# Optimization experiments

Measured on AMD Instinct MI355X. Metric: run time of the kernel, lower is better.

Reference implementation:

```python
import jax, jax.numpy as jnp
import numpy as np
from jax import lax

CAPACITY_FACTOR = 1.0

def setup_inputs() -> dict:
    key = jax.random.key(0)
    k1, k2 = jax.random.split(key)
    x = jax.random.normal(k1, (16384, 4096), dtype=jnp.float32)
    wg = jax.random.normal(k2, (128, 4096), dtype=jnp.float32) * (1.0 / np.sqrt(4096))
    return {"x": x, "wg": wg}


def reference(x, wg):
    # logits: [T, E]
    logits = jnp.einsum('td,ed->te', x, wg)
    T, E = logits.shape
    capacity = 2 * int(CAPACITY_FACTOR * ((T + E - 1) // E))  # static python int

    # top-2 expert indices per token
    _, top2 = lax.top_k(logits, 2)           # [T, 2]
    idx1, idx2 = top2[:, 0], top2[:, 1]       # [T]

    mask1 = jax.nn.one_hot(idx1, E, dtype=jnp.int32)  # [T, E]
    mask2 = jax.nn.one_hot(idx2, E, dtype=jnp.int32)

    gates = jax.nn.softmax(logits, axis=1)    # [T, E]
    gates1_s = jnp.sum(gates * mask1, axis=1)  # [T]
    gates2_s = jnp.sum(gates * mask2, axis=1)

    # per-expert running position (cumsum over tokens)
    locations1 = jnp.cumsum(mask1, axis=0) - 1
    locations2 = jnp.cumsum(mask2, axis=0) - 1 + jnp.sum(mask1, axis=0, keepdims=True)

    # drop tokens over capacity
    mask1 = mask1 * (locations1 < capacity).astype(jnp.int32)
    mask2 = mask2 * (locations2 < capacity).astype(jnp.int32)

    locations1_s = jnp.sum(locations1 * mask1, axis=1)  # [T]
    locations2_s = jnp.sum(locations2 * mask2, axis=1)

    # load-balancing aux loss (float32 branch of original)
    me = jnp.sum(gates, axis=0)                       # [E]
    ce = jnp.sum(mask1.astype(gates.dtype), axis=0)   # [E] (post-capacity mask)
    l_aux = jnp.sum(me * ce) * (E / (T * T))

    return (l_aux, capacity, E,
            idx1.astype(jnp.int32), idx2.astype(jnp.int32),
            locations1_s.astype(jnp.int32), locations2_s.astype(jnp.int32),
            gates1_s, gates2_s)
```

## Files before the change

kernel.cpp:

```cpp
#include <hip/hip_runtime.h>

typedef _Float16 half8 __attribute__((ext_vector_type(8)));
typedef _Float16 half4 __attribute__((ext_vector_type(4)));
typedef float    f32x4 __attribute__((ext_vector_type(4)));

#define T_TOK 16384
#define D_DIM 4096
#define E_EXP 128
#define CAP   256
#define BM    64
#define NT    32

#define A_BUF_SZ  16384
#define A_PIPE_SZ 32768

__global__ __launch_bounds__(256) void prep_wt(
    const float* __restrict__ wg, _Float16* __restrict__ wt)
{
    const int t = blockIdx.x * 256 + threadIdx.x;
    const int c = t & 3;
    const int e = (t >> 2) & 127;
    const int s = t >> 9;

    const float* src = wg + (size_t)e * D_DIM + s * 32 + c * 8;
    const f32x4 v0 = *reinterpret_cast<const f32x4*>(src);
    const f32x4 v1 = *reinterpret_cast<const f32x4*>(src + 4);

    half8 h, m;
#pragma unroll
    for (int j = 0; j < 4; j++) {
        float sv = v0[j] * 64.0f;
        _Float16 hh = (_Float16)sv;
        h[j] = hh; m[j] = (_Float16)(sv - (float)hh);
        sv = v1[j] * 64.0f;
        hh = (_Float16)sv;
        h[4 + j] = hh; m[4 + j] = (_Float16)(sv - (float)hh);
    }
    _Float16* dst = wt + (size_t)s * 8192 + e * 32 + c * 8;
    *reinterpret_cast<half8*>(dst)        = h;
    *reinterpret_cast<half8*>(dst + 4096) = m;
}

__global__ __launch_bounds__(1024, 4) void gemm_gate(
    const float* __restrict__ x, const _Float16* __restrict__ wt,
    float* __restrict__ out, float* __restrict__ me, int* __restrict__ cnt1)
{
    __shared__ char smem[2 * A_PIPE_SZ];

    const int tid  = threadIdx.x;
    const int row0 = blockIdx.x * BM;
    const int lane = tid & 63;
    const int w    = tid >> 6;
    const int kp   = w >> 3;
    const int wl   = w & 7;
    const int lr   = lane & 15;
    const int lq   = lane >> 4;

    const int sp   = tid >> 9;
    const int srow = (tid >> 3) & 63;
    const int sg   = tid & 7;
    const float* xA = x + (size_t)(row0 + srow) * D_DIM + sp * 2048 + sg * 8;
    const int awr_h = sp * A_PIPE_SZ + srow * 256 + (sg >> 2) * 128 +
                      (((sg & 3)    ) ^ (srow & 7)) * 16;
    const int awr_m = sp * A_PIPE_SZ + srow * 256 + (sg >> 2) * 128 +
                      (((sg & 3) | 4) ^ (srow & 7)) * 16;

    const int ah_ch = ((lq    ) ^ (lr & 7)) * 16;
    const int am_ch = ((lq | 4) ^ (lr & 7)) * 16;
    const char* const ard = smem + kp * A_PIPE_SZ;

    const _Float16* const wtB =
        wt + (size_t)(kp * 64) * 8192 + (wl * 16 + lr) * 32 + lq * 8;

    f32x4 acc[4];
#pragma unroll
    for (int i = 0; i < 4; i++) acc[i] = (f32x4)0.0f;

#define CONV_WRITE(a0, a1, buf)                                               \
    {                                                                         \
        half8 h, m;                                                           \
        _Pragma("unroll") for (int j = 0; j < 4; j++) {                       \
            _Float16 hh = (_Float16)a0[j];                                    \
            h[j] = hh; m[j] = (_Float16)(a0[j] - (float)hh);                  \
            hh = (_Float16)a1[j];                                             \
            h[4 + j] = hh; m[4 + j] = (_Float16)(a1[j] - (float)hh);          \
        }                                                                     \
        char* const wb = smem + (buf) * A_BUF_SZ;                             \
        *reinterpret_cast<half8*>(wb + awr_h) = h;                            \
        *reinterpret_cast<half8*>(wb + awr_m) = m;                            \
    }

#define BAR()                                                                 \
    asm volatile("s_waitcnt lgkmcnt(0)" ::: "memory");                        \
    __builtin_amdgcn_sched_barrier(0);                                        \
    __builtin_amdgcn_s_barrier();                                             \
    __builtin_amdgcn_sched_barrier(0);

#define SUBSTEP(cur, ks, t)                                                   \
    {                                                                         \
        const _Float16* bp = wtB + (size_t)((2 * (t) + (ks)) & 63) * 8192;    \
        const half8 Bh = *reinterpret_cast<const half8*>(bp);                 \
        const half8 Bm = *reinterpret_cast<const half8*>(bp + 4096);          \
        half8 Ah[4], Am[4];                                                   \
        _Pragma("unroll") for (int rf = 0; rf < 4; rf++) {                    \
            const char* ab = ard + (cur) * A_BUF_SZ +                         \
                             (rf * 16 + lr) * 256 + (ks) * 128;               \
            Ah[rf] = *reinterpret_cast<const half8*>(ab + ah_ch);             \
            Am[rf] = *reinterpret_cast<const half8*>(ab + am_ch);             \
        }                                                                     \
        _Pragma("unroll") for (int rf = 0; rf < 4; rf++) {                    \
            acc[rf] = __builtin_amdgcn_mfma_f32_16x16x32_f16(                 \
                Am[rf], Bh, acc[rf], 0, 0, 0);                                \
            acc[rf] = __builtin_amdgcn_mfma_f32_16x16x32_f16(                 \
                Ah[rf], Bm, acc[rf], 0, 0, 0);                                \
            acc[rf] = __builtin_amdgcn_mfma_f32_16x16x32_f16(                 \
                Ah[rf], Bh, acc[rf], 0, 0, 0);                                \
        }                                                                     \
    }

#define STEP(cur, t)                                                          \
    {                                                                         \
        const int kn = (((t) + 1) & (NT - 1)) * 64;                           \
        const f32x4 a0 = *reinterpret_cast<const f32x4*>(xA + kn);            \
        const f32x4 a1 = *reinterpret_cast<const f32x4*>(xA + kn + 4);        \
        SUBSTEP(cur, 0, t);                                                   \
        SUBSTEP(cur, 1, t);                                                   \
        CONV_WRITE(a0, a1, (cur) ^ 1);                                        \
        BAR();                                                                \
    }

    {
        const f32x4 a0 = *reinterpret_cast<const f32x4*>(xA);
        const f32x4 a1 = *reinterpret_cast<const f32x4*>(xA + 4);
        CONV_WRITE(a0, a1, 0);
        BAR();
    }

    for (int t = 0; t < NT; t += 2) {
        STEP(0, t);
        STEP(1, t + 1);
    }

#undef STEP
#undef SUBSTEP
#undef BAR
#undef CONV_WRITE

    float* lg = reinterpret_cast<float*>(smem);
    if (kp == 1) {
#pragma unroll
        for (int rf = 0; rf < 4; rf++)
#pragma unroll
            for (int r = 0; r < 4; r++)
                lg[(rf * 16 + lq * 4 + r) * 129 + wl * 16 + lr] =
                    acc[rf][r] * 0.015625f;
    }
    __syncthreads();
    if (kp == 0) {
#pragma unroll
        for (int rf = 0; rf < 4; rf++)
#pragma unroll
            for (int r = 0; r < 4; r++)
                lg[(rf * 16 + lq * 4 + r) * 129 + wl * 16 + lr] +=
                    acc[rf][r] * 0.015625f;
    }
    __syncthreads();

    if (tid < BM) {
        const int r = tid;
        const int t = row0 + r;
        float m1 = -1e30f, m2 = -1e30f;
        int   i1 = 0, i2 = 0;
        for (int e = 0; e < E_EXP; e++) {
            const float v = lg[r * 129 + e];
            if (v > m1)      { m2 = m1; i2 = i1; m1 = v; i1 = e; }
            else if (v > m2) { m2 = v; i2 = e; }
        }
        float s = 0.0f;
        for (int e = 0; e < E_EXP; e++) s += __expf(lg[r * 129 + e] - m1);
        const float inv = 1.0f / s;

        out[3 + 0 * T_TOK + t] = (float)i1;
        out[3 + 1 * T_TOK + t] = (float)i2;
        out[3 + 4 * T_TOK + t] = inv;
        out[3 + 5 * T_TOK + t] = __expf(m2 - m1) * inv;
        atomicAdd(&cnt1[i1], 1);

        for (int e = 0; e < E_EXP; e++)
            lg[r * 129 + e] = __expf(lg[r * 129 + e] - m1) * inv;
    }
    __syncthreads();

    if (tid < E_EXP) {
        float s = 0.0f;
        for (int r = 0; r < BM; r++) s += lg[r * 129 + tid];
        atomicAdd(&me[tid], s);
    }
}

__global__ __launch_bounds__(1024) void rank_kernel(
    float* __restrict__ out, const int* __restrict__ cnt1)
{
    const int  e      = blockIdx.x & 127;
    const bool second = blockIdx.x >= 128;
    const int  tid    = threadIdx.x;
    const int  lane   = tid & 63;
    const int  w      = tid >> 6;

    __shared__ int wtot[16];

    const float* idxA = out + 3 + (second ? T_TOK : 0);
    float* loc = out + 3 + (second ? 3 * T_TOK : 2 * T_TOK);

    const unsigned long long below = (1ull << lane) - 1ull;
    int base = second ? cnt1[e] : 0;

    for (int t0 = 0; t0 < T_TOK; t0 += 1024) {
        const int t = t0 + tid;
        const int f = ((int)idxA[t] == e);
        const unsigned long long m = __ballot(f);
        const int pre = __popcll(m & below);
        const int tot = __popcll(m);
        if (lane == 0) wtot[w] = tot;
        __syncthreads();
        int off = 0, all = 0;
#pragma unroll
        for (int i = 0; i < 16; i++) {
            const int v = wtot[i];
            if (i < w) off += v;
            all += v;
        }
        if (f) {
            const int rank = base + off + pre;
            loc[t] = (rank < CAP) ? (float)rank : 0.0f;
        }
        base += all;
        __syncthreads();
    }
}

__global__ __launch_bounds__(128) void finalize_kernel(
    const float* __restrict__ me, const int* __restrict__ cnt1,
    float* __restrict__ out)
{
    __shared__ float red[2];
    const int tid = threadIdx.x;
    const int c = cnt1[tid];
    float p = me[tid] * (float)((c < CAP) ? c : CAP);
#pragma unroll
    for (int o = 32; o > 0; o >>= 1) p += __shfl_down(p, o);
    if ((tid & 63) == 0) red[tid >> 6] = p;
    __syncthreads();
    if (tid == 0) {
        const float tot = red[0] + red[1];
        out[0] = tot * ((float)E_EXP / ((float)T_TOK * (float)T_TOK));
        out[1] = (float)CAP;
        out[2] = (float)E_EXP;
    }
}

extern "C" void kernel_launch(void* const* d_in, const int* in_sizes, int n_in,
                              void* d_out, int out_size, void* d_ws, size_t ws_size,
                              hipStream_t stream)
{
    const float* x  = (const float*)d_in[0];
    const float* wg = (const float*)d_in[1];
    float* out = (float*)d_out;

    float* me   = (float*)d_ws;
    int*   cnt1 = (int*)((char*)d_ws + 512);
    _Float16* wt = (_Float16*)((char*)d_ws + 1024);

    hipMemsetAsync(d_ws, 0, 1024, stream);
    prep_wt<<<256, 256, 0, stream>>>(wg, wt);
    gemm_gate<<<T_TOK / BM, 1024, 0, stream>>>(x, wt, out, me, cnt1);
    rank_kernel<<<2 * E_EXP, 1024, 0, stream>>>(out, cnt1);
    finalize_kernel<<<1, 128, 0, stream>>>(me, cnt1, out);
}
```

Before: 118.3 us.

## Switch gate GEMM to 32x32 MFMA tiles with 32-row blocks and B prefetch

Restructures the gating GEMM to use 32x32x16 MFMA instructions, with each wave owning a 32x32 output tile, and halves the token block to 32 rows with 512 threads. That doubles the block count for better occupancy and cuts shared memory use. B fragments are register-prefetched one step ahead, and the softmax normalisation pass is spread across all threads instead of 32. Each block now reloads the full weight matrix for fewer rows, so global/L2 traffic for the weights doubles, and register pressure rises from the prefetched B values.

New measurement: 130.7 us. +10.5%, slower.

```diff
diff --git a/kernel.cpp b/kernel.cpp
--- a/kernel.cpp
+++ b/kernel.cpp
@@ -1,18 +1,19 @@
 #include <hip/hip_runtime.h>
 
-typedef _Float16 half8 __attribute__((ext_vector_type(8)));
-typedef _Float16 half4 __attribute__((ext_vector_type(4)));
-typedef float    f32x4 __attribute__((ext_vector_type(4)));
+typedef _Float16 half8  __attribute__((ext_vector_type(8)));
+typedef float    f32x4  __attribute__((ext_vector_type(4)));
+typedef float    f32x16 __attribute__((ext_vector_type(16)));
 
 #define T_TOK 16384
 #define D_DIM 4096
 #define E_EXP 128
 #define CAP   256
-#define BM    64
+#define BM    32
 #define NT    32
 
-#define A_BUF_SZ  16384
-#define A_PIPE_SZ 32768
+#define A_BUF   8192
+#define A_PIPE  16384
+#define SMEM_SZ 33792
 
 __global__ __launch_bounds__(256) void prep_wt(
     const float* __restrict__ wg, _Float16* __restrict__ wt)
@@ -41,40 +42,42 @@
     *reinterpret_cast<half8*>(dst + 4096) = m;
 }
 
-__global__ __launch_bounds__(1024, 4) void gemm_gate(
+__global__ __launch_bounds__(512, 4) void gemm_gate(
     const float* __restrict__ x, const _Float16* __restrict__ wt,
     float* __restrict__ out, float* __restrict__ me, int* __restrict__ cnt1)
 {
-    __shared__ char smem[2 * A_PIPE_SZ];
+    __shared__ char smem[SMEM_SZ];
 
     const int tid  = threadIdx.x;
     const int row0 = blockIdx.x * BM;
     const int lane = tid & 63;
     const int w    = tid >> 6;
-    const int kp   = w >> 3;
-    const int wl   = w & 7;
-    const int lr   = lane & 15;
-    const int lq   = lane >> 4;
-
-    const int sp   = tid >> 9;
-    const int srow = (tid >> 3) & 63;
-    const int sg   = tid & 7;
-    const float* xA = x + (size_t)(row0 + srow) * D_DIM + sp * 2048 + sg * 8;
-    const int awr_h = sp * A_PIPE_SZ + srow * 256 + (sg >> 2) * 128 +
-                      (((sg & 3)    ) ^ (srow & 7)) * 16;
-    const int awr_m = sp * A_PIPE_SZ + srow * 256 + (sg >> 2) * 128 +
-                      (((sg & 3) | 4) ^ (srow & 7)) * 16;
-
-    const int ah_ch = ((lq    ) ^ (lr & 7)) * 16;
-    const int am_ch = ((lq | 4) ^ (lr & 7)) * 16;
-    const char* const ard = smem + kp * A_PIPE_SZ;
+    const int kp   = w >> 2;
+    const int wl   = w & 3;
+    const int col  = lane & 31;
+    const int k8   = lane >> 5;
+
+    const int sp = tid >> 8;
+    const int sr = (tid >> 3) & 31;
+    const int sg = tid & 7;
+    const float* xA = x + (size_t)(row0 + sr) * D_DIM + sp * 2048 + sg * 8;
+    const int awr_h = sp * A_PIPE + sr * 256 + ((sg ^ (sr & 7)) * 16);
+
+    const char* const ard = smem + kp * A_PIPE + col * 256;
+    const int rsw = col & 7;
 
     const _Float16* const wtB =
-        wt + (size_t)(kp * 64) * 8192 + (wl * 16 + lr) * 32 + lq * 8;
-
-    f32x4 acc[4];
-#pragma unroll
-    for (int i = 0; i < 4; i++) acc[i] = (f32x4)0.0f;
+        wt + (size_t)(kp * 64) * 8192 + (wl * 32 + col) * 32 + k8 * 8;
+
+    f32x16 acc = (f32x16)0.0f;
+
+#define LOAD_BS(Bh, Bm, t, k)                                                 \
+    {                                                                         \
+        const _Float16* bp = wtB +                                            \
+            (size_t)((2 * (t) + ((k) >> 1)) & 63) * 8192 + ((k) & 1) * 16;    \
+        Bh = *reinterpret_cast<const half8*>(bp);                             \
+        Bm = *reinterpret_cast<const half8*>(bp + 4096);                      \
+    }
 
 #define CONV_WRITE(a0, a1, buf)                                               \
     {                                                                         \
@@ -85,9 +88,9 @@
             hh = (_Float16)a1[j];                                             \
             h[4 + j] = hh; m[4 + j] = (_Float16)(a1[j] - (float)hh);          \
         }                                                                     \
-        char* const wb = smem + (buf) * A_BUF_SZ;                             \
-        *reinterpret_cast<half8*>(wb + awr_h) = h;                            \
-        *reinterpret_cast<half8*>(wb + awr_m) = m;                            \
+        char* const wb = smem + (buf) * A_BUF + awr_h;                        \
+        *reinterpret_cast<half8*>(wb)       = h;                              \
+        *reinterpret_cast<half8*>(wb + 128) = m;                              \
     }
 
 #define BAR()                                                                 \
@@ -96,42 +99,41 @@
     __builtin_amdgcn_s_barrier();                                             \
     __builtin_amdgcn_sched_barrier(0);
 
-#define SUBSTEP(cur, ks, t)                                                   \
-    {                                                                         \
-        const _Float16* bp = wtB + (size_t)((2 * (t) + (ks)) & 63) * 8192;    \
-        const half8 Bh = *reinterpret_cast<const half8*>(bp);                 \
-        const half8 Bm = *reinterpret_cast<const half8*>(bp + 4096);          \
-        half8 Ah[4], Am[4];                                                   \
-        _Pragma("unroll") for (int rf = 0; rf < 4; rf++) {                    \
-            const char* ab = ard + (cur) * A_BUF_SZ +                         \
-                             (rf * 16 + lr) * 256 + (ks) * 128;               \
-            Ah[rf] = *reinterpret_cast<const half8*>(ab + ah_ch);             \
-            Am[rf] = *reinterpret_cast<const half8*>(ab + am_ch);             \
-        }                                                                     \
-        _Pragma("unroll") for (int rf = 0; rf < 4; rf++) {                    \
-            acc[rf] = __builtin_amdgcn_mfma_f32_16x16x32_f16(                 \
-                Am[rf], Bh, acc[rf], 0, 0, 0);                                \
-            acc[rf] = __builtin_amdgcn_mfma_f32_16x16x32_f16(                 \
-                Ah[rf], Bm, acc[rf], 0, 0, 0);                                \
-            acc[rf] = __builtin_amdgcn_mfma_f32_16x16x32_f16(                 \
-                Ah[rf], Bh, acc[rf], 0, 0, 0);                                \
-        }                                                                     \
+#define SUB(cur, k, Bh, Bm)                                                   \
+    {                                                                         \
+        const char* ab = ard + (cur) * A_BUF + ((((k) * 2 + k8) ^ rsw) * 16); \
+        const half8 Ah = *reinterpret_cast<const half8*>(ab);                 \
+        const half8 Am = *reinterpret_cast<const half8*>(ab + 128);           \
+        acc = __builtin_amdgcn_mfma_f32_32x32x16_f16(Am, Bh, acc, 0, 0, 0);   \
+        acc = __builtin_amdgcn_mfma_f32_32x32x16_f16(Ah, Bm, acc, 0, 0, 0);   \
+        acc = __builtin_amdgcn_mfma_f32_32x32x16_f16(Ah, Bh, acc, 0, 0, 0);   \
     }
 
 #define STEP(cur, t)                                                          \
     {                                                                         \
+        LOAD_BS(B1h, B1m, t, 1);                                              \
+        LOAD_BS(B2h, B2m, t, 2);                                              \
+        LOAD_BS(B3h, B3m, t, 3);                                              \
+        __builtin_amdgcn_sched_barrier(0);                                    \
         const int kn = (((t) + 1) & (NT - 1)) * 64;                           \
         const f32x4 a0 = *reinterpret_cast<const f32x4*>(xA + kn);            \
         const f32x4 a1 = *reinterpret_cast<const f32x4*>(xA + kn + 4);        \
-        SUBSTEP(cur, 0, t);                                                   \
-        SUBSTEP(cur, 1, t);                                                   \
+        __builtin_amdgcn_sched_barrier(0);                                    \
+        SUB(cur, 0, B0h, B0m);                                                \
+        LOAD_BS(B0h, B0m, (t) + 1, 0);                                        \
+        SUB(cur, 1, B1h, B1m);                                                \
+        SUB(cur, 2, B2h, B2m);                                                \
+        SUB(cur, 3, B3h, B3m);                                                \
         CONV_WRITE(a0, a1, (cur) ^ 1);                                        \
         BAR();                                                                \
     }
+
+    half8 B0h, B0m, B1h, B1m, B2h, B2m, B3h, B3m;
 
     {
         const f32x4 a0 = *reinterpret_cast<const f32x4*>(xA);
         const f32x4 a1 = *reinterpret_cast<const f32x4*>(xA + 4);
+        LOAD_BS(B0h, B0m, 0, 0);
         CONV_WRITE(a0, a1, 0);
         BAR();
     }
@@ -142,29 +144,31 @@
     }
 
 #undef STEP
-#undef SUBSTEP
+#undef SUB
 #undef BAR
 #undef CONV_WRITE
+#undef LOAD_BS
 
     float* lg = reinterpret_cast<float*>(smem);
     if (kp == 1) {
 #pragma unroll
-        for (int rf = 0; rf < 4; rf++)
-#pragma unroll
-            for (int r = 0; r < 4; r++)
-                lg[(rf * 16 + lq * 4 + r) * 129 + wl * 16 + lr] =
-                    acc[rf][r] * 0.015625f;
+        for (int reg = 0; reg < 16; reg++) {
+            const int row = (reg & 3) + 8 * (reg >> 2) + 4 * k8;
+            lg[row * 129 + wl * 32 + col] = acc[reg] * 0.015625f;
+        }
     }
     __syncthreads();
     if (kp == 0) {
 #pragma unroll
-        for (int rf = 0; rf < 4; rf++)
-#pragma unroll
-            for (int r = 0; r < 4; r++)
-                lg[(rf * 16 + lq * 4 + r) * 129 + wl * 16 + lr] +=
-                    acc[rf][r] * 0.015625f;
-    }
-    __syncthreads();
+        for (int reg = 0; reg < 16; reg++) {
+            const int row = (reg & 3) + 8 * (reg >> 2) + 4 * k8;
+            lg[row * 129 + wl * 32 + col] += acc[reg] * 0.015625f;
+        }
+    }
+    __syncthreads();
+
+    float* sm1v  = reinterpret_cast<float*>(smem + 20480);
+    float* sinvv = sm1v + 32;
 
     if (tid < BM) {
         const int r = tid;
@@ -185,9 +189,18 @@
         out[3 + 4 * T_TOK + t] = inv;
         out[3 + 5 * T_TOK + t] = __expf(m2 - m1) * inv;
         atomicAdd(&cnt1[i1], 1);
-
-        for (int e = 0; e < E_EXP; e++)
-            lg[r * 129 + e] = __expf(lg[r * 129 + e] - m1) * inv;
+        sm1v[r]  = m1;
+        sinvv[r] = inv;
+    }
+    __syncthreads();
+
+    {
+        const int r  = tid & 31;
+        const int e0 = (tid >> 5) * 8;
+        const float m1 = sm1v[r], inv = sinvv[r];
+#pragma unroll
+        for (int j = 0; j < 8; j++)
+            lg[r * 129 + e0 + j] = __expf(lg[r * 129 + e0 + j] - m1) * inv;
     }
     __syncthreads();
 
@@ -273,7 +286,7 @@
 
     hipMemsetAsync(d_ws, 0, 1024, stream);
     prep_wt<<<256, 256, 0, stream>>>(wg, wt);
-    gemm_gate<<<T_TOK / BM, 1024, 0, stream>>>(x, wt, out, me, cnt1);
+    gemm_gate<<<T_TOK / BM, 512, 0, stream>>>(x, wt, out, me, cnt1);
     rank_kernel<<<2 * E_EXP, 1024, 0, stream>>>(out, cnt1);
     finalize_kernel<<<1, 128, 0, stream>>>(me, cnt1, out);
 }
```
